# Optimization experiments

Hardware: AMD Instinct MI355X
Metric: run time of the kernel (lower is better)

The kernel has to match this reference:

```python
import jax, jax.numpy as jnp
import numpy as np

K = 7
PAD = 3  # k==7 branch
SIGMA_SPACE = 5.0
SIGMA_COLOR = 0.1


def _gkern2d(k, sig):
    # torch: arange(-k//2 + 1.0, k//2 + 1.0) -> [-3, ..., 3] for k=7
    ax = jnp.arange(-(k // 2) + 0.0, k // 2 + 1.0, dtype=jnp.float32)
    xx, yy = jnp.meshgrid(ax, ax, indexing='ij')
    return jnp.exp(-(xx ** 2 + yy ** 2) / (2.0 * sig ** 2))  # (k, k)


def setup_inputs() -> dict:
    key = jax.random.key(0)
    I = jax.random.uniform(key, (2, 1, 720, 1280), dtype=jnp.float32)
    return {"I": I}


def reference(I) -> jnp.ndarray:
    n, c, h, w = I.shape  # c == 1
    g = _gkern2d(K, SIGMA_SPACE).reshape(1, K * K, 1, 1)  # spatial Gaussian weights
    Ip = jnp.pad(I, ((0, 0), (0, 0), (PAD, PAD), (PAD, PAD)))
    # Shift: k*k shifted views stacked on channel dim -> (n, k*k, h, w)
    Is = jnp.concatenate(
        [Ip[:, :, y:y + h, x:x + w] for y in range(K) for x in range(K)], axis=1
    )
    Is = jax.lax.stop_gradient(Is)  # original uses .data (detached)
    D = (Is - I) ** 2  # I broadcasts over the k*k shift dim (expand in torch)
    Dd = jnp.exp(-D / (2.0 * SIGMA_COLOR ** 2)) * g
    W_denom = jnp.sum(Dd, axis=1)          # (n, h, w)
    If = jnp.sum(Dd * Is, axis=1) / W_denom  # (n, h, w)
    return If
```

## Files before the change

### kernel.cpp

```cpp
#include <hip/hip_runtime.h>

#define IMG_H 720
#define IMG_W 1280
#define HW (IMG_H * IMG_W)

#define TX 32
#define TY 16
#define NBX (IMG_W / TX)
#define NBY (IMG_H / TY)
#define NBLK (NBX * NBY)
#define LW2 40
#define LH (TY + 6)

#define KSCALE 8.493218148592486f
#define INVK   0.11774100235949044f
#define S2SCALE 0.028853900817779268f

typedef float f2 __attribute__((ext_vector_type(2)));

#if defined(__has_builtin)
#if __has_builtin(__builtin_amdgcn_exp2f)
#define EXP2(x) __builtin_amdgcn_exp2f(x)
#else
#define EXP2(x) exp2f(x)
#endif
#if __has_builtin(__builtin_amdgcn_rcpf)
#define RCP(x) __builtin_amdgcn_rcpf(x)
#else
#define RCP(x) (1.0f / (x))
#endif
#else
#define EXP2(x) exp2f(x)
#define RCP(x) (1.0f / (x))
#endif

__device__ constexpr int MIDX[19] = {0, 1, 2, -1, 3, 4, -1, -1, 5, 6,
                                     7, -1, -1, 8, -1, -1, -1, -1, 9};

__device__ __forceinline__ void tap(f2 v, f2 nck, f2 s2p, f2& aw, f2& aiw) {
    f2 dd = v + nck;
    f2 e = __builtin_elementwise_fma(dd, dd, s2p);
    f2 w;
    w.x = EXP2(-e.x);
    w.y = EXP2(-e.y);
    aw += w;
    aiw = __builtin_elementwise_fma(w, v, aiw);
}

template <int RY2>
__device__ __forceinline__ void do_row_t(const f2* __restrict__ rowptr,
                                         f2 nck0, f2 nck1,
                                         f2& aw0, f2& aiw0, f2& aw1, f2& aiw1,
                                         const f2 (&s2)[10]) {
    f2 f[8];
    *(float4*)(&f[0]) = *(const float4*)(rowptr + 0);
    *(float4*)(&f[2]) = *(const float4*)(rowptr + 2);
    *(float4*)(&f[4]) = *(const float4*)(rowptr + 4);
    *(float4*)(&f[6]) = *(const float4*)(rowptr + 6);
#pragma unroll
    for (int dx = 0; dx < 7; ++dx) {
        const int sidx = MIDX[RY2 + (dx - 3) * (dx - 3)];
        tap(f[dx], nck0, s2[sidx], aw0, aiw0);
        tap(f[dx + 1], nck1, s2[sidx], aw1, aiw1);
    }
}

__global__ __launch_bounds__(256, 8) void bilateral_pk(
    const float* __restrict__ I, float* __restrict__ O) {
    int b = blockIdx.x;
    int bx = b % NBX, by = b / NBX;
    int tx0 = bx * TX, ty0 = by * TY;
    int tid = threadIdx.x;

    __shared__ f2 S[LH][LW2];
    const float* img0 = I;
    const float* img1 = I + HW;

    bool interior = (bx >= 1) && (bx <= NBX - 2) && (by >= 1) && (by <= NBY - 2);
    if (interior) {
        if (tid < LH * (LW2 / 4)) {
            int r = tid / (LW2 / 4), q = tid % (LW2 / 4);
            int gy = ty0 - 3 + r, gx = tx0 - 3 + q * 4;
            float4 a0 = *(const float4*)(img0 + gy * IMG_W + gx);
            float4 a1 = *(const float4*)(img1 + gy * IMG_W + gx);
            float4 w0, w1;
            w0.x = a0.x * KSCALE; w0.y = a1.x * KSCALE;
            w0.z = a0.y * KSCALE; w0.w = a1.y * KSCALE;
            w1.x = a0.z * KSCALE; w1.y = a1.z * KSCALE;
            w1.z = a0.w * KSCALE; w1.w = a1.w * KSCALE;
            *(float4*)(&S[r][q * 4]) = w0;
            *(float4*)(&S[r][q * 4 + 2]) = w1;
        }
    } else {
#pragma unroll
        for (int i = 0; i < 4; ++i) {
            int idx = tid + i * 256;
            if (idx < LH * LW2) {
                int r = idx / LW2, c = idx % LW2;
                int gy = ty0 - 3 + r, gx = tx0 - 3 + c;
                float v0 = 0.f, v1 = 0.f;
                if (gy >= 0 && gy < IMG_H && gx >= 0 && gx < IMG_W) {
                    v0 = img0[gy * IMG_W + gx];
                    v1 = img1[gy * IMG_W + gx];
                }
                f2 t = {v0 * KSCALE, v1 * KSCALE};
                S[r][c] = t;
            }
        }
    }
    __syncthreads();

    const float sv[10] = {0.f, 1.f, 2.f, 4.f, 5.f, 8.f, 9.f, 10.f, 13.f, 18.f};
    f2 s2reg[10];
#pragma unroll
    for (int j = 0; j < 10; ++j) {
        float s = sv[j] * S2SCALE;
        s2reg[j].x = s;
        s2reg[j].y = s;
        asm("" : "+v"(s2reg[j]));
    }

    int px = tid & 15;
    int py = tid >> 4;
    int x0 = px * 2;

    f2 aw0 = {0.f, 0.f}, aw1 = {0.f, 0.f};
    f2 aiw0 = {0.f, 0.f}, aiw1 = {0.f, 0.f};
    f2 nck0, nck1;

    {
        const f2* rowptr = &S[py + 3][x0];
        f2 f[8];
        *(float4*)(&f[0]) = *(const float4*)(rowptr + 0);
        *(float4*)(&f[2]) = *(const float4*)(rowptr + 2);
        *(float4*)(&f[4]) = *(const float4*)(rowptr + 4);
        *(float4*)(&f[6]) = *(const float4*)(rowptr + 6);
        nck0 = -f[3];
        nck1 = -f[4];
#pragma unroll
        for (int dx = 0; dx < 7; ++dx) {
            const int sidx = MIDX[(dx - 3) * (dx - 3)];
            tap(f[dx], nck0, s2reg[sidx], aw0, aiw0);
            tap(f[dx + 1], nck1, s2reg[sidx], aw1, aiw1);
        }
    }
    do_row_t<9>(&S[py + 0][x0], nck0, nck1, aw0, aiw0, aw1, aiw1, s2reg);
    do_row_t<4>(&S[py + 1][x0], nck0, nck1, aw0, aiw0, aw1, aiw1, s2reg);
    do_row_t<1>(&S[py + 2][x0], nck0, nck1, aw0, aiw0, aw1, aiw1, s2reg);
    do_row_t<1>(&S[py + 4][x0], nck0, nck1, aw0, aiw0, aw1, aiw1, s2reg);
    do_row_t<4>(&S[py + 5][x0], nck0, nck1, aw0, aiw0, aw1, aiw1, s2reg);
    do_row_t<9>(&S[py + 6][x0], nck0, nck1, aw0, aiw0, aw1, aiw1, s2reg);

    int oy = ty0 + py;
    float2 r0, r1;
    r0.x = aiw0.x * RCP(aw0.x) * INVK;
    r0.y = aiw1.x * RCP(aw1.x) * INVK;
    r1.x = aiw0.y * RCP(aw0.y) * INVK;
    r1.y = aiw1.y * RCP(aw1.y) * INVK;
    *(float2*)(O + (size_t)oy * IMG_W + tx0 + x0) = r0;
    *(float2*)(O + HW + (size_t)oy * IMG_W + tx0 + x0) = r1;
}

extern "C" void kernel_launch(void* const* d_in, const int* in_sizes, int n_in,
                              void* d_out, int out_size, void* d_ws, size_t ws_size,
                              hipStream_t stream) {
    const float* I = (const float*)d_in[0];
    float* O = (float*)d_out;
    bilateral_pk<<<NBLK, 256, 0, stream>>>(I, O);
}
```

Baseline: 19.45 us.

## Compute four horizontal pixels per thread with wider 64x8 tiles and 128-thread blocks

Each thread now produces four adjacent output pixels instead of two. This cuts shared-memory row loads per output, since 10 loaded values serve 4 pixels × 7 taps. The tile becomes 64x8 with 128-thread blocks, thread mapping changes to py-fastest, and outputs are written as float4. The asm barrier that pinned the sigma constants in registers is removed. Register pressure and LDS bank patterns change, which may reduce occupancy or cause bank conflicts.

Measured after the change: 22.37 us. 15.0% more time.

```diff
diff --git a/kernel.cpp b/kernel.cpp
--- a/kernel.cpp
+++ b/kernel.cpp
@@ -4,13 +4,13 @@
 #define IMG_W 1280
 #define HW (IMG_H * IMG_W)
 
-#define TX 32
-#define TY 16
-#define NBX (IMG_W / TX)
-#define NBY (IMG_H / TY)
+#define TXP 64
+#define TYR 8
+#define NBX (IMG_W / TXP)
+#define NBY (IMG_H / TYR)
 #define NBLK (NBX * NBY)
-#define LW2 40
-#define LH (TY + 6)
+#define LW2 74
+#define LH (TYR + 6)
 
 #define KSCALE 8.493218148592486f
 #define INVK   0.11774100235949044f
@@ -48,28 +48,29 @@
 }
 
 template <int RY2>
-__device__ __forceinline__ void do_row_t(const f2* __restrict__ rowptr,
-                                         f2 nck0, f2 nck1,
-                                         f2& aw0, f2& aiw0, f2& aw1, f2& aiw1,
-                                         const f2 (&s2)[10]) {
-    f2 f[8];
+__device__ __forceinline__ void do_row4(const f2* __restrict__ rowptr,
+                                        const f2 (&nck)[4], f2 (&aw)[4],
+                                        f2 (&aiw)[4], const f2 (&s2)[10]) {
+    f2 f[10];
     *(float4*)(&f[0]) = *(const float4*)(rowptr + 0);
     *(float4*)(&f[2]) = *(const float4*)(rowptr + 2);
     *(float4*)(&f[4]) = *(const float4*)(rowptr + 4);
     *(float4*)(&f[6]) = *(const float4*)(rowptr + 6);
+    *(float4*)(&f[8]) = *(const float4*)(rowptr + 8);
 #pragma unroll
     for (int dx = 0; dx < 7; ++dx) {
         const int sidx = MIDX[RY2 + (dx - 3) * (dx - 3)];
-        tap(f[dx], nck0, s2[sidx], aw0, aiw0);
-        tap(f[dx + 1], nck1, s2[sidx], aw1, aiw1);
+#pragma unroll
+        for (int j = 0; j < 4; ++j)
+            tap(f[dx + j], nck[j], s2[sidx], aw[j], aiw[j]);
     }
 }
 
-__global__ __launch_bounds__(256, 8) void bilateral_pk(
+__global__ __launch_bounds__(128, 8) void bilateral_pk4(
     const float* __restrict__ I, float* __restrict__ O) {
     int b = blockIdx.x;
     int bx = b % NBX, by = b / NBX;
-    int tx0 = bx * TX, ty0 = by * TY;
+    int tx0 = bx * TXP, ty0 = by * TYR;
     int tid = threadIdx.x;
 
     __shared__ f2 S[LH][LW2];
@@ -78,87 +79,98 @@
 
     bool interior = (bx >= 1) && (bx <= NBX - 2) && (by >= 1) && (by <= NBY - 2);
     if (interior) {
-        if (tid < LH * (LW2 / 4)) {
-            int r = tid / (LW2 / 4), q = tid % (LW2 / 4);
-            int gy = ty0 - 3 + r, gx = tx0 - 3 + q * 4;
-            float4 a0 = *(const float4*)(img0 + gy * IMG_W + gx);
-            float4 a1 = *(const float4*)(img1 + gy * IMG_W + gx);
-            float4 w0, w1;
-            w0.x = a0.x * KSCALE; w0.y = a1.x * KSCALE;
-            w0.z = a0.y * KSCALE; w0.w = a1.y * KSCALE;
-            w1.x = a0.z * KSCALE; w1.y = a1.z * KSCALE;
-            w1.z = a0.w * KSCALE; w1.w = a1.w * KSCALE;
-            *(float4*)(&S[r][q * 4]) = w0;
-            *(float4*)(&S[r][q * 4 + 2]) = w1;
+#pragma unroll
+        for (int i = 0; i < 2; ++i) {
+            int id = tid + i * 128;
+            if (id < LH * 18) {
+                int r = id / 18, q = id % 18;
+                int gy = ty0 - 3 + r, gx = tx0 - 3 + q * 4;
+                float4 a0 = *(const float4*)(img0 + gy * IMG_W + gx);
+                float4 a1 = *(const float4*)(img1 + gy * IMG_W + gx);
+                float4 w0, w1;
+                w0.x = a0.x * KSCALE; w0.y = a1.x * KSCALE;
+                w0.z = a0.y * KSCALE; w0.w = a1.y * KSCALE;
+                w1.x = a0.z * KSCALE; w1.y = a1.z * KSCALE;
+                w1.z = a0.w * KSCALE; w1.w = a1.w * KSCALE;
+                *(float4*)(&S[r][q * 4]) = w0;
+                *(float4*)(&S[r][q * 4 + 2]) = w1;
+            }
         }
     } else {
 #pragma unroll
-        for (int i = 0; i < 4; ++i) {
-            int idx = tid + i * 256;
+        for (int i = 0; i < 9; ++i) {
+            int idx = tid + i * 128;
             if (idx < LH * LW2) {
                 int r = idx / LW2, c = idx % LW2;
-                int gy = ty0 - 3 + r, gx = tx0 - 3 + c;
-                float v0 = 0.f, v1 = 0.f;
-                if (gy >= 0 && gy < IMG_H && gx >= 0 && gx < IMG_W) {
-                    v0 = img0[gy * IMG_W + gx];
-                    v1 = img1[gy * IMG_W + gx];
+                if (c < 70) {
+                    int gy = ty0 - 3 + r, gx = tx0 - 3 + c;
+                    float v0 = 0.f, v1 = 0.f;
+                    if (gy >= 0 && gy < IMG_H && gx >= 0 && gx < IMG_W) {
+                        v0 = img0[gy * IMG_W + gx];
+                        v1 = img1[gy * IMG_W + gx];
+                    }
+                    f2 t = {v0 * KSCALE, v1 * KSCALE};
+                    S[r][c] = t;
                 }
-                f2 t = {v0 * KSCALE, v1 * KSCALE};
-                S[r][c] = t;
             }
         }
     }
     __syncthreads();
 
     const float sv[10] = {0.f, 1.f, 2.f, 4.f, 5.f, 8.f, 9.f, 10.f, 13.f, 18.f};
-    f2 s2reg[10];
+    f2 s2c[10];
 #pragma unroll
     for (int j = 0; j < 10; ++j) {
         float s = sv[j] * S2SCALE;
-        s2reg[j].x = s;
-        s2reg[j].y = s;
-        asm("" : "+v"(s2reg[j]));
+        s2c[j].x = s;
+        s2c[j].y = s;
     }
 
-    int px = tid & 15;
-    int py = tid >> 4;
-    int x0 = px * 2;
+    int py = tid & 7;
+    int px = tid >> 3;
+    int x0 = px * 4;
 
-    f2 aw0 = {0.f, 0.f}, aw1 = {0.f, 0.f};
-    f2 aiw0 = {0.f, 0.f}, aiw1 = {0.f, 0.f};
-    f2 nck0, nck1;
+    f2 aw[4] = {{0.f, 0.f}, {0.f, 0.f}, {0.f, 0.f}, {0.f, 0.f}};
+    f2 aiw[4] = {{0.f, 0.f}, {0.f, 0.f}, {0.f, 0.f}, {0.f, 0.f}};
+    f2 nck[4];
 
     {
         const f2* rowptr = &S[py + 3][x0];
-        f2 f[8];
+        f2 f[10];
         *(float4*)(&f[0]) = *(const float4*)(rowptr + 0);
         *(float4*)(&f[2]) = *(const float4*)(rowptr + 2);
         *(float4*)(&f[4]) = *(const float4*)(rowptr + 4);
         *(float4*)(&f[6]) = *(const float4*)(rowptr + 6);
-        nck0 = -f[3];
-        nck1 = -f[4];
+        *(float4*)(&f[8]) = *(const float4*)(rowptr + 8);
+#pragma unroll
+        for (int j = 0; j < 4; ++j) nck[j] = -f[3 + j];
 #pragma unroll
         for (int dx = 0; dx < 7; ++dx) {
             const int sidx = MIDX[(dx - 3) * (dx - 3)];
-            tap(f[dx], nck0, s2reg[sidx], aw0, aiw0);
-            tap(f[dx + 1], nck1, s2reg[sidx], aw1, aiw1);
+#pragma unroll
+            for (int j = 0; j < 4; ++j)
+                tap(f[dx + j], nck[j], s2c[sidx], aw[j], aiw[j]);
         }
     }
-    do_row_t<9>(&S[py + 0][x0], nck0, nck1, aw0, aiw0, aw1, aiw1, s2reg);
-    do_row_t<4>(&S[py + 1][x0], nck0, nck1, aw0, aiw0, aw1, aiw1, s2reg);
-    do_row_t<1>(&S[py + 2][x0], nck0, nck1, aw0, aiw0, aw1, aiw1, s2reg);
-    do_row_t<1>(&S[py + 4][x0], nck0, nck1, aw0, aiw0, aw1, aiw1, s2reg);
-    do_row_t<4>(&S[py + 5][x0], nck0, nck1, aw0, aiw0, aw1, aiw1, s2reg);
-    do_row_t<9>(&S[py + 6][x0], nck0, nck1, aw0, aiw0, aw1, aiw1, s2reg);
+    do_row4<9>(&S[py + 0][x0], nck, aw, aiw, s2c);
+    do_row4<4>(&S[py + 1][x0], nck, aw, aiw, s2c);
+    do_row4<1>(&S[py + 2][x0], nck, aw, aiw, s2c);
+    do_row4<1>(&S[py + 4][x0], nck, aw, aiw, s2c);
+    do_row4<4>(&S[py + 5][x0], nck, aw, aiw, s2c);
+    do_row4<9>(&S[py + 6][x0], nck, aw, aiw, s2c);
 
     int oy = ty0 + py;
-    float2 r0, r1;
-    r0.x = aiw0.x * RCP(aw0.x) * INVK;
-    r0.y = aiw1.x * RCP(aw1.x) * INVK;
-    r1.x = aiw0.y * RCP(aw0.y) * INVK;
-    r1.y = aiw1.y * RCP(aw1.y) * INVK;
-    *(float2*)(O + (size_t)oy * IMG_W + tx0 + x0) = r0;
-    *(float2*)(O + HW + (size_t)oy * IMG_W + tx0 + x0) = r1;
+    float4 r0, r1;
+    r0.x = aiw[0].x * RCP(aw[0].x) * INVK;
+    r0.y = aiw[1].x * RCP(aw[1].x) * INVK;
+    r0.z = aiw[2].x * RCP(aw[2].x) * INVK;
+    r0.w = aiw[3].x * RCP(aw[3].x) * INVK;
+    r1.x = aiw[0].y * RCP(aw[0].y) * INVK;
+    r1.y = aiw[1].y * RCP(aw[1].y) * INVK;
+    r1.z = aiw[2].y * RCP(aw[2].y) * INVK;
+    r1.w = aiw[3].y * RCP(aw[3].y) * INVK;
+    *(float4*)(O + (size_t)oy * IMG_W + tx0 + x0) = r0;
+    *(float4*)(O + HW + (size_t)oy * IMG_W + tx0 + x0) = r1;
 }
 
 extern "C" void kernel_launch(void* const* d_in, const int* in_sizes, int n_in,
@@ -166,5 +178,5 @@
                               hipStream_t stream) {
     const float* I = (const float*)d_in[0];
     float* O = (float*)d_out;
-    bilateral_pk<<<NBLK, 256, 0, stream>>>(I, O);
+    bilateral_pk4<<<NBLK, 128, 0, stream>>>(I, O);
 }
```
